# Optimization experiments

Hardware: AMD Instinct MI355X
Metric: run time of the kernel (lower is better)

The kernel has to match this reference:

```python
import jax, jax.numpy as jnp
import numpy as np

NB_NEIGHBORS = 16
RADIUS = 0.25
SPLIT = 32
FEATURE_SIZE = 128
FEATS = (256, 128, 32)
N = 50000


def setup_inputs() -> dict:
    key = jax.random.key(0)
    ks = jax.random.split(key, 12)
    def lin(k, fan_in, fan_out):
        bound = 1.0 / np.sqrt(fan_in)
        kw, kb = jax.random.split(k)
        W = jax.random.uniform(kw, (fan_in, fan_out), jnp.float32, -bound, bound)
        b = jax.random.uniform(kb, (fan_out,), jnp.float32, -bound, bound)
        return W, b
    points = jax.random.normal(ks[0], (N, 3), jnp.float32)
    features = jax.random.normal(ks[1], (N, SPLIT + FEATURE_SIZE), jnp.float32)
    batch = jnp.sort(jax.random.randint(ks[2], (N,), 0, 32, jnp.int64))
    # neighborhood decoder modeled as linear: split -> nb_neighbors*3
    W_nbh, b_nbh = lin(ks[3], SPLIT, NB_NEIGHBORS * 3)
    W1, b1 = lin(ks[4], FEATURE_SIZE + 3, FEATS[0])
    W2, b2 = lin(ks[5], FEATS[0], FEATS[1])
    W3, b3 = lin(ks[6], FEATS[1], FEATS[2])
    return {"points": points, "features": features, "batch": batch,
            "W_nbh": W_nbh, "b_nbh": b_nbh,
            "W1": W1, "b1": b1, "W2": W2, "b2": b2, "W3": W3, "b3": b3}


def reference(points, features, batch, W_nbh, b_nbh, W1, b1, W2, b2, W3, b3):
    point_features = features[:, :SPLIT]            # [N, split]
    feature_features = features[:, SPLIT:]          # [N, feature_size]
    # neighborhood decoder: per-point relative offsets for nb_neighbors points
    relative_points = (point_features @ W_nbh + b_nbh).reshape(-1, 3)  # [N*nb, 3]
    output_batch = jnp.repeat(batch, NB_NEIGHBORS)                     # [N*nb]
    features_repeated = jnp.repeat(feature_features, NB_NEIGHBORS, axis=0)  # [N*nb, fs]
    concat = jnp.concatenate([relative_points, features_repeated], axis=1)  # [N*nb, fs+3]
    h = jax.nn.relu(concat @ W1 + b1)
    h = jax.nn.relu(h @ W2 + b2)
    fc3_features = jax.nn.relu(h @ W3 + b3)
    anchor_points = jnp.repeat(points, NB_NEIGHBORS, axis=0)  # [N*nb, 3]
    output_points = anchor_points + relative_points * RADIUS
    return (output_points, fc3_features, output_batch)
```

## Files before the change

kernel.cpp:

```cpp
#include <hip/hip_runtime.h>


#define NPTS 50000
#define MROWS (NPTS * 16)
#define OFF_FC3 ((size_t)MROWS * 3)
#define OFF_BATCH ((size_t)MROWS * 35)

typedef unsigned int uint_;
typedef unsigned short ushort_;
typedef __attribute__((ext_vector_type(8))) short bf16x8s;
typedef __attribute__((ext_vector_type(16))) float f32x16;

#define MFMA(a, b, c) __builtin_amdgcn_mfma_f32_32x32x16_bf16(a, b, c, 0, 0, 0)
#define CROW(r, h) (((r) & 3) + 8 * ((r) >> 2) + 4 * (h))

#define WS_W2T 0
#define WS_W3T 32768
#define WS_W1PT 36864
#define WS_WNT 69632
#define WS_S 71680
#define WS_REL_BYTES 25743360

__device__ __forceinline__ float bl(uint_ u) { return __uint_as_float(u << 16); }
__device__ __forceinline__ float bh(uint_ u) { return __uint_as_float(u & 0xffff0000u); }
__device__ __forceinline__ ushort_ f2b(float f) {
  uint_ u = __float_as_uint(f);
  u += 0x7fffu + ((u >> 16) & 1u);
  return (ushort_)(u >> 16);
}
__device__ __forceinline__ uint_ cvtpk(float lo, float hi) {
  uint_ r;
  asm("v_cvt_pk_bf16_f32 %0, %1, %2" : "=v"(r) : "v"(lo), "v"(hi));
  return r;
}
__device__ __forceinline__ float relu_(float x) { return fmaxf(x, 0.f); }

template<bool F32>
__device__ __forceinline__ float ldv(const void* p, int i) {
  if (F32) return ((const float*)p)[i];
  return bl((uint_)((const ushort_*)p)[i]);
}

struct F8 { float v[8]; };
template<bool F32>
__device__ __forceinline__ F8 ld8(const void* p, int idx) {
  F8 r;
  if (F32) {
    float4 a = *(const float4*)((const float*)p + idx);
    float4 b = *(const float4*)((const float*)p + idx + 4);
    r.v[0] = a.x; r.v[1] = a.y; r.v[2] = a.z; r.v[3] = a.w;
    r.v[4] = b.x; r.v[5] = b.y; r.v[6] = b.z; r.v[7] = b.w;
  } else {
    uint4 u = *(const uint4*)((const ushort_*)p + idx);
    r.v[0] = bl(u.x); r.v[1] = bh(u.x); r.v[2] = bl(u.y); r.v[3] = bh(u.y);
    r.v[4] = bl(u.z); r.v[5] = bh(u.z); r.v[6] = bl(u.w); r.v[7] = bh(u.w);
  }
  return r;
}
template<bool F32>
__device__ __forceinline__ void ld4f(const void* p, int idx, float* o) {
  if (F32) {
    float4 v = *(const float4*)((const float*)p + idx);
    o[0] = v.x; o[1] = v.y; o[2] = v.z; o[3] = v.w;
  } else {
    uint2 v = *(const uint2*)((const ushort_*)p + idx);
    o[0] = bl(v.x); o[1] = bh(v.x); o[2] = bl(v.y); o[3] = bh(v.y);
  }
}

union FragU { uint_ u[4]; uint4 q; bf16x8s v; };
__device__ __forceinline__ bf16x8s pack8(const F8& f) {
  FragU o;
  #pragma unroll
  for (int j = 0; j < 4; ++j) o.u[j] = cvtpk(f.v[2 * j], f.v[2 * j + 1]);
  return o.v;
}

__device__ __forceinline__ bool sniff_f32(const void* feats) {
  const ushort_* u = (const ushort_*)feats;
  int pass = 0;
  #pragma unroll 8
  for (int m = 0; m < 32; ++m) {
    int ex = (u[m] >> 7) & 0xff;
    pass += (ex >= 100 && ex <= 140) ? 1 : 0;
  }
  return pass < 28;
}

__global__ void __launch_bounds__(256)
kT(const void* features, const void* batch, const void* W1, const void* Wn,
   const void* W2, const void* W3, ushort_* wsu, float* out) {
  bool f32 = sniff_f32(features);
  const uint_* bu = (const uint_*)batch;
  int nz = 0;
  #pragma unroll
  for (int m = 0; m < 16; ++m) nz += (bu[49999 - 2 * m] != 0u) ? 1 : 0;
  bool i64 = (nz == 0);

  const int total = 32768 + 32768 + 4096 + 2048 + 800000;
  for (int i = blockIdx.x * 256 + threadIdx.x; i < total; i += gridDim.x * 256) {
    if (i < 32768) {
      int n = i & 255, k = i >> 8;
      wsu[WS_W1PT + n * 128 + k] = f32 ? f2b(((const float*)W1)[(3 + k) * 256 + n])
                                       : ((const ushort_*)W1)[(3 + k) * 256 + n];
    } else if (i < 65536) {
      int i2 = i - 32768, n = i2 & 127, k = i2 >> 7;
      wsu[WS_W2T + n * 256 + k] = f32 ? f2b(((const float*)W2)[k * 128 + n])
                                      : ((const ushort_*)W2)[k * 128 + n];
    } else if (i < 69632) {
      int i3 = i - 65536, n = i3 & 31, k = i3 >> 5;
      wsu[WS_W3T + n * 128 + k] = f32 ? f2b(((const float*)W3)[k * 32 + n])
                                      : ((const ushort_*)W3)[k * 32 + n];
    } else if (i < 71680) {
      int i4 = i - 69632, n = i4 >> 5, k = i4 & 31;
      ushort_ v = 0;
      if (n < 48) v = f32 ? f2b(((const float*)Wn)[k * 48 + n])
                          : ((const ushort_*)Wn)[k * 48 + n];
      wsu[WS_WNT + n * 32 + k] = v;
    } else {
      int g = i - 71680;
      int idx = g >> 4;
      int v = i64 ? (int)bu[2 * idx] : ((const int*)batch)[idx];
      out[OFF_BATCH + (size_t)g] = (float)v;
    }
  }
}

template<bool F32>
__device__ void runS(const void* points, const void* features, const void* bn,
                     const void* b1, ushort_* wsu, float* out,
                     ushort_* w1pt, ushort_* feats) {
  const ushort_* W1pT_ws = wsu + WS_W1PT;
  const ushort_* WnT_ws = wsu + WS_WNT;
  ushort_* S_ws = wsu + WS_S;
  float* rel_ws = (float*)((char*)wsu + WS_REL_BYTES);
  const int tid = threadIdx.x;

  for (int c = tid; c < 4096; c += 256) {
    int n = c >> 4, s = c & 15;
    uint4 src = *(const uint4*)(W1pT_ws + c * 8);
    *(uint4*)((char*)w1pt + n * 256 + ((s * 16) ^ ((n & 7) << 4))) = src;
  }

  const int w = tid >> 6, lane = tid & 63, l31 = lane & 31, h = lane >> 5, h8 = h * 8;
  const int mt = w & 1, ctb = (w >> 1) * 4, ctr = w >> 1;

  for (int tile = blockIdx.x; tile < 782; tile += 512) {
    const int pbase = tile * 64;
    for (int c = tid; c < 2048; c += 256) {
      int row = c >> 5, c4 = c & 31;
      int p = pbase + row;
      uint2 d = {0u, 0u};
      if (p < NPTS) {
        if (F32) {
          float4 v = *(const float4*)((const float*)features + p * 160 + 32 + c4 * 4);
          d.x = cvtpk(v.x, v.y); d.y = cvtpk(v.z, v.w);
        } else {
          d = *(const uint2*)((const ushort_*)features + p * 160 + 32 + c4 * 4);
        }
      }
      *(uint2*)((char*)feats + row * 256 + ((c4 * 8) ^ ((row & 7) << 4))) = d;
    }
    __syncthreads();

    bf16x8s af[8];
    #pragma unroll
    for (int ks = 0; ks < 8; ++ks) {
      int row = mt * 32 + l31;
      af[ks] = *(const bf16x8s*)((const char*)feats + row * 256 +
                                 (((ks * 16 + h8) * 2) ^ ((row & 7) << 4)));
    }
    #pragma unroll
    for (int ci = 0; ci < 4; ++ci) {
      int ct = ctb + ci;
      float b1v = ldv<F32>(b1, ct * 32 + l31);
      f32x16 acc;
      #pragma unroll
      for (int r = 0; r < 16; ++r) acc[r] = b1v;
      #pragma unroll
      for (int ks = 0; ks < 8; ++ks) {
        int n = ct * 32 + l31;
        bf16x8s bf = *(const bf16x8s*)((const char*)w1pt + n * 256 +
                                       (((ks * 16 + h8) * 2) ^ ((n & 7) << 4)));
        acc = MFMA(af[ks], bf, acc);
      }
      #pragma unroll
      for (int r = 0; r < 16; ++r) {
        int p = pbase + mt * 32 + CROW(r, h);
        if (p < NPTS) S_ws[p * 256 + ct * 32 + l31] = f2b(acc[r]);
      }
    }

    {
      int pm = pbase + mt * 32 + l31;
      pm = pm < NPTS ? pm : NPTS - 1;
      bf16x8s ar[2];
      #pragma unroll
      for (int ks = 0; ks < 2; ++ks) {
        F8 v = ld8<F32>(features, pm * 160 + ks * 16 + h8);
        ar[ks] = pack8(v);
      }
      f32x16 acc;
      #pragma unroll
      for (int r = 0; r < 16; ++r) acc[r] = 0.f;
      #pragma unroll
      for (int ks = 0; ks < 2; ++ks) {
        int n = ctr * 32 + l31;
        FragU bw;
        bw.q = *(const uint4*)(WnT_ws + n * 32 + ks * 16 + h8);
        acc = MFMA(ar[ks], bw.v, acc);
      }
      int j = ctr * 32 + l31;
      if (j < 48) {
        float bnv = ldv<F32>(bn, j);
        int c = j - (j / 3) * 3;
        #pragma unroll
        for (int r = 0; r < 16; ++r) {
          int p = pbase + mt * 32 + CROW(r, h);
          if (p < NPTS) {
            float rv = acc[r] + bnv;
            rel_ws[p * 48 + j] = rv;
            out[(size_t)p * 48 + j] = ldv<F32>(points, p * 3 + c) + 0.25f * rv;
          }
        }
      }
    }
    __syncthreads();
  }
}

__global__ void __launch_bounds__(256, 2)
kS(const void* points, const void* features, const void* bn, const void* b1,
   ushort_* wsu, float* out) {
  __shared__ ushort_ w1pt[32768];
  __shared__ ushort_ feats[8192];
  if (sniff_f32(features))
    runS<true>(points, features, bn, b1, wsu, out, w1pt, feats);
  else
    runS<false>(points, features, bn, b1, wsu, out, w1pt, feats);
}

__device__ __forceinline__ bf16x8s build8(uint4 s, const F8& wx, const F8& wy,
                                          const F8& wz, float r0, float r1, float r2) {
  uint_ su[4] = {s.x, s.y, s.z, s.w};
  F8 f;
  #pragma unroll
  for (int j = 0; j < 8; ++j) {
    uint_ u = su[j >> 1];
    float sv = (j & 1) ? bh(u) : bl(u);
    f.v[j] = relu_(sv + r0 * wx.v[j] + r1 * wy.v[j] + r2 * wz.v[j]);
  }
  return pack8(f);
}

__device__ __forceinline__ bf16x8s assemble(const f32x16& a, int base, bool lo) {
  float e[8];
  #pragma unroll
  for (int j = 0; j < 8; ++j) e[j] = relu_(a[base + j]);
  uint_ A0 = cvtpk(e[0], e[1]), A1 = cvtpk(e[2], e[3]);
  uint_ B0 = cvtpk(e[4], e[5]), B1 = cvtpk(e[6], e[7]);
  uint_ sA0 = (uint_)__shfl_xor((int)A0, 32);
  uint_ sA1 = (uint_)__shfl_xor((int)A1, 32);
  uint_ sB0 = (uint_)__shfl_xor((int)B0, 32);
  uint_ sB1 = (uint_)__shfl_xor((int)B1, 32);
  FragU o;
  o.u[0] = lo ? A0 : sB0;
  o.u[1] = lo ? A1 : sB1;
  o.u[2] = lo ? sA0 : B0;
  o.u[3] = lo ? sA1 : B1;
  return o.v;
}

template<bool F32>
__device__ void runM(const void* W1, const void* b2, const void* b3,
                     const ushort_* wsu, float* out,
                     ushort_* w2t, ushort_* w3t) {
  const ushort_* S_ws = wsu + WS_S;
  const float* rel_ws = (const float*)((const char*)wsu + WS_REL_BYTES);
  const int tid = threadIdx.x;

  for (int c = tid; c < 4608; c += 256) {
    if (c < 4096) {
      int n = c >> 5, s = c & 31;
      uint4 src = *(const uint4*)(wsu + WS_W2T + c * 8);
      *(uint4*)((char*)w2t + n * 512 + ((s * 16) ^ ((n & 7) << 4))) = src;
    } else {
      int c2 = c - 4096, n = c2 >> 4, s = c2 & 15;
      uint4 src = *(const uint4*)(wsu + WS_W3T + c2 * 8);
      *(uint4*)((char*)w3t + n * 256 + ((s * 16) ^ ((n & 7) << 4))) = src;
    }
  }
  __syncthreads();

  const int w = tid >> 6, lane = tid & 63, l31 = lane & 31, h = lane >> 5;
  const int h8 = h * 8, nb = lane & 15;
  const bool lo = lane < 32;
  const int slot = blockIdx.x * 4 + w;

  for (int g = slot; g < 12500; g += 2048) {
    const int p0 = g * 4;
    const int pA = p0 + (l31 >> 4), pB = pA + 2;
    const float rA0 = rel_ws[pA * 48 + nb * 3 + 0];
    const float rA1 = rel_ws[pA * 48 + nb * 3 + 1];
    const float rA2 = rel_ws[pA * 48 + nb * 3 + 2];
    const float rB0 = rel_ws[pB * 48 + nb * 3 + 0];
    const float rB1 = rel_ws[pB * 48 + nb * 3 + 1];
    const float rB2 = rel_ws[pB * 48 + nb * 3 + 2];

    f32x16 accA[4], accB[4];
    #pragma unroll
    for (int mt = 0; mt < 4; ++mt) {
      #pragma unroll
      for (int q = 0; q < 4; ++q) {
        float t[4];
        ld4f<F32>(b2, mt * 32 + q * 8 + 4 * h, t);
        #pragma unroll
        for (int s = 0; s < 4; ++s) {
          accA[mt][4 * q + s] = t[s];
          accB[mt][4 * q + s] = t[s];
        }
      }
    }

    #pragma unroll 1
    for (int kh = 0; kh < 2; ++kh) {
      bf16x8s hA[8], hB[8];
      #pragma unroll
      for (int ks = 0; ks < 8; ++ks) {
        int koff = kh * 128 + ks * 16 + h8;
        F8 wx = ld8<F32>(W1, koff);
        F8 wy = ld8<F32>(W1, 256 + koff);
        F8 wz = ld8<F32>(W1, 512 + koff);
        uint4 sa = *(const uint4*)(S_ws + pA * 256 + koff);
        uint4 sb = *(const uint4*)(S_ws + pB * 256 + koff);
        hA[ks] = build8(sa, wx, wy, wz, rA0, rA1, rA2);
        hB[ks] = build8(sb, wx, wy, wz, rB0, rB1, rB2);
      }
      #pragma unroll
      for (int ks = 0; ks < 8; ++ks) {
        int kb = (kh * 128 + ks * 16 + h8) * 2;
        #pragma unroll
        for (int mt = 0; mt < 4; ++mt) {
          int n = mt * 32 + l31;
          bf16x8s af = *(const bf16x8s*)((const char*)w2t + n * 512 +
                                         (kb ^ ((n & 7) << 4)));
          accA[mt] = MFMA(af, hA[ks], accA[mt]);
          accB[mt] = MFMA(af, hB[ks], accB[mt]);
        }
      }
    }

    f32x16 o3A, o3B;
    #pragma unroll
    for (int q = 0; q < 4; ++q) {
      float t[4];
      ld4f<F32>(b3, q * 8 + 4 * h, t);
      #pragma unroll
      for (int s = 0; s < 4; ++s) {
        o3A[4 * q + s] = t[s];
        o3B[4 * q + s] = t[s];
      }
    }
    #pragma unroll
    for (int ks3 = 0; ks3 < 8; ++ks3) {
      int kb = (ks3 * 16 + h8) * 2;
      bf16x8s a3 = *(const bf16x8s*)((const char*)w3t + l31 * 256 +
                                     (kb ^ ((l31 & 7) << 4)));
      const int mt = ks3 >> 1, base = (ks3 & 1) * 8;
      bf16x8s B3A = assemble(accA[mt], base, lo);
      bf16x8s B3B = assemble(accB[mt], base, lo);
      o3A = MFMA(a3, B3A, o3A);
      o3B = MFMA(a3, B3B, o3B);
    }

    const size_t rowA = (size_t)p0 * 16 + l31;
    #pragma unroll
    for (int q = 0; q < 4; ++q) {
      float4 vA = {relu_(o3A[4 * q]), relu_(o3A[4 * q + 1]),
                   relu_(o3A[4 * q + 2]), relu_(o3A[4 * q + 3])};
      float4 vB = {relu_(o3B[4 * q]), relu_(o3B[4 * q + 1]),
                   relu_(o3B[4 * q + 2]), relu_(o3B[4 * q + 3])};
      *(float4*)(out + OFF_FC3 + rowA * 32 + q * 8 + 4 * h) = vA;
      *(float4*)(out + OFF_FC3 + (rowA + 32) * 32 + q * 8 + 4 * h) = vB;
    }
  }
}

__global__ void __launch_bounds__(256, 2)
kM(const void* features, const void* W1, const void* b2, const void* b3,
   const ushort_* wsu, float* out) {
  __shared__ ushort_ w2t[32768];
  __shared__ ushort_ w3t[4096];
  if (sniff_f32(features))
    runM<true>(W1, b2, b3, wsu, out, w2t, w3t);
  else
    runM<false>(W1, b2, b3, wsu, out, w2t, w3t);
}

extern "C" void kernel_launch(void* const* d_in, const int* in_sizes, int n_in,
                              void* d_out, int out_size, void* d_ws, size_t ws_size,
                              hipStream_t stream) {
  const void* points   = d_in[0];
  const void* features = d_in[1];
  const void* batch    = d_in[2];
  const void* Wn = d_in[3];  const void* bn = d_in[4];
  const void* W1 = d_in[5];  const void* b1 = d_in[6];
  const void* W2 = d_in[7];  const void* b2 = d_in[8];
  const void* W3 = d_in[9];  const void* b3 = d_in[10];
  float* out = (float*)d_out;
  ushort_* wsu = (ushort_*)d_ws;

  hipLaunchKernelGGL(kT, dim3(512), dim3(256), 0, stream,
                     features, batch, W1, Wn, W2, W3, wsu, out);
  hipLaunchKernelGGL(kS, dim3(512), dim3(256), 0, stream,
                     points, features, bn, b1, wsu, out);
  hipLaunchKernelGGL(kM, dim3(512), dim3(256), 0, stream,
                     features, W1, b2, b3, wsu, out);
}
```

Baseline: 160.0 us.

## Halve per-wave work in MLP kernel, use 512-thread blocks, stage W1 rows in LDS

The fused fc2/fc3 kernel now has each wave process 2 points (32 rows) instead of 4, and uses 512-thread blocks, so accumulator register pressure drops and more waves can be resident per CU. The three W1 coordinate rows are copied once into shared memory instead of being read from global memory in the inner loop. The kS grid is raised to 782 so each tile gets its own block. The cost is that each W2 fragment read from LDS now feeds one MFMA instead of two, which doubles LDS read traffic per output row.

```diff
diff --git a/kernel.cpp b/kernel.cpp
--- a/kernel.cpp
+++ b/kernel.cpp
@@ -55,6 +55,14 @@
     r.v[0] = bl(u.x); r.v[1] = bh(u.x); r.v[2] = bl(u.y); r.v[3] = bh(u.y);
     r.v[4] = bl(u.z); r.v[5] = bh(u.z); r.v[6] = bl(u.w); r.v[7] = bh(u.w);
   }
+  return r;
+}
+__device__ __forceinline__ F8 ld8lds(const float* p) {
+  F8 r;
+  float4 a = *(const float4*)p;
+  float4 b = *(const float4*)(p + 4);
+  r.v[0] = a.x; r.v[1] = a.y; r.v[2] = a.z; r.v[3] = a.w;
+  r.v[4] = b.x; r.v[5] = b.y; r.v[6] = b.z; r.v[7] = b.w;
   return r;
 }
 template<bool F32>
@@ -145,7 +153,7 @@
   const int w = tid >> 6, lane = tid & 63, l31 = lane & 31, h = lane >> 5, h8 = h * 8;
   const int mt = w & 1, ctb = (w >> 1) * 4, ctr = w >> 1;
 
-  for (int tile = blockIdx.x; tile < 782; tile += 512) {
+  for (int tile = blockIdx.x; tile < 782; tile += gridDim.x) {
     const int pbase = tile * 64;
     for (int c = tid; c < 2048; c += 256) {
       int row = c >> 5, c4 = c & 31;
@@ -274,12 +282,12 @@
 template<bool F32>
 __device__ void runM(const void* W1, const void* b2, const void* b3,
                      const ushort_* wsu, float* out,
-                     ushort_* w2t, ushort_* w3t) {
+                     ushort_* w2t, ushort_* w3t, float* w1f) {
   const ushort_* S_ws = wsu + WS_S;
   const float* rel_ws = (const float*)((const char*)wsu + WS_REL_BYTES);
   const int tid = threadIdx.x;
 
-  for (int c = tid; c < 4608; c += 256) {
+  for (int c = tid; c < 4608; c += 512) {
     if (c < 4096) {
       int n = c >> 5, s = c & 31;
       uint4 src = *(const uint4*)(wsu + WS_W2T + c * 8);
@@ -290,24 +298,22 @@
       *(uint4*)((char*)w3t + n * 256 + ((s * 16) ^ ((n & 7) << 4))) = src;
     }
   }
+  for (int c = tid; c < 768; c += 512) w1f[c] = ldv<F32>(W1, c);
   __syncthreads();
 
   const int w = tid >> 6, lane = tid & 63, l31 = lane & 31, h = lane >> 5;
   const int h8 = h * 8, nb = lane & 15;
   const bool lo = lane < 32;
-  const int slot = blockIdx.x * 4 + w;
-
-  for (int g = slot; g < 12500; g += 2048) {
-    const int p0 = g * 4;
-    const int pA = p0 + (l31 >> 4), pB = pA + 2;
-    const float rA0 = rel_ws[pA * 48 + nb * 3 + 0];
-    const float rA1 = rel_ws[pA * 48 + nb * 3 + 1];
-    const float rA2 = rel_ws[pA * 48 + nb * 3 + 2];
-    const float rB0 = rel_ws[pB * 48 + nb * 3 + 0];
-    const float rB1 = rel_ws[pB * 48 + nb * 3 + 1];
-    const float rB2 = rel_ws[pB * 48 + nb * 3 + 2];
-
-    f32x16 accA[4], accB[4];
+  const int slot = blockIdx.x * 8 + w;
+
+  for (int g = slot; g < 25000; g += 4096) {
+    const int p0 = g * 2;
+    const int p = p0 + (l31 >> 4);
+    const float r0 = rel_ws[p * 48 + nb * 3 + 0];
+    const float r1 = rel_ws[p * 48 + nb * 3 + 1];
+    const float r2 = rel_ws[p * 48 + nb * 3 + 2];
+
+    f32x16 acc[4];
     #pragma unroll
     for (int mt = 0; mt < 4; ++mt) {
       #pragma unroll
@@ -315,86 +321,65 @@
         float t[4];
         ld4f<F32>(b2, mt * 32 + q * 8 + 4 * h, t);
         #pragma unroll
-        for (int s = 0; s < 4; ++s) {
-          accA[mt][4 * q + s] = t[s];
-          accB[mt][4 * q + s] = t[s];
-        }
-      }
-    }
-
-    #pragma unroll 1
-    for (int kh = 0; kh < 2; ++kh) {
-      bf16x8s hA[8], hB[8];
-      #pragma unroll
-      for (int ks = 0; ks < 8; ++ks) {
-        int koff = kh * 128 + ks * 16 + h8;
-        F8 wx = ld8<F32>(W1, koff);
-        F8 wy = ld8<F32>(W1, 256 + koff);
-        F8 wz = ld8<F32>(W1, 512 + koff);
-        uint4 sa = *(const uint4*)(S_ws + pA * 256 + koff);
-        uint4 sb = *(const uint4*)(S_ws + pB * 256 + koff);
-        hA[ks] = build8(sa, wx, wy, wz, rA0, rA1, rA2);
-        hB[ks] = build8(sb, wx, wy, wz, rB0, rB1, rB2);
-      }
-      #pragma unroll
-      for (int ks = 0; ks < 8; ++ks) {
-        int kb = (kh * 128 + ks * 16 + h8) * 2;
-        #pragma unroll
-        for (int mt = 0; mt < 4; ++mt) {
-          int n = mt * 32 + l31;
-          bf16x8s af = *(const bf16x8s*)((const char*)w2t + n * 512 +
-                                         (kb ^ ((n & 7) << 4)));
-          accA[mt] = MFMA(af, hA[ks], accA[mt]);
-          accB[mt] = MFMA(af, hB[ks], accB[mt]);
-        }
-      }
-    }
-
-    f32x16 o3A, o3B;
+        for (int s = 0; s < 4; ++s) acc[mt][4 * q + s] = t[s];
+      }
+    }
+
+    #pragma unroll 2
+    for (int ks = 0; ks < 16; ++ks) {
+      const int koff = ks * 16 + h8;
+      F8 wx = ld8lds(w1f + koff);
+      F8 wy = ld8lds(w1f + 256 + koff);
+      F8 wz = ld8lds(w1f + 512 + koff);
+      uint4 sa = *(const uint4*)(S_ws + p * 256 + koff);
+      bf16x8s hh = build8(sa, wx, wy, wz, r0, r1, r2);
+      const int kb = koff * 2;
+      #pragma unroll
+      for (int mt = 0; mt < 4; ++mt) {
+        int n = mt * 32 + l31;
+        bf16x8s af = *(const bf16x8s*)((const char*)w2t + n * 512 +
+                                       (kb ^ ((n & 7) << 4)));
+        acc[mt] = MFMA(af, hh, acc[mt]);
+      }
+    }
+
+    f32x16 o3;
     #pragma unroll
     for (int q = 0; q < 4; ++q) {
       float t[4];
       ld4f<F32>(b3, q * 8 + 4 * h, t);
       #pragma unroll
-      for (int s = 0; s < 4; ++s) {
-        o3A[4 * q + s] = t[s];
-        o3B[4 * q + s] = t[s];
-      }
+      for (int s = 0; s < 4; ++s) o3[4 * q + s] = t[s];
     }
     #pragma unroll
     for (int ks3 = 0; ks3 < 8; ++ks3) {
       int kb = (ks3 * 16 + h8) * 2;
       bf16x8s a3 = *(const bf16x8s*)((const char*)w3t + l31 * 256 +
                                      (kb ^ ((l31 & 7) << 4)));
-      const int mt = ks3 >> 1, base = (ks3 & 1) * 8;
-      bf16x8s B3A = assemble(accA[mt], base, lo);
-      bf16x8s B3B = assemble(accB[mt], base, lo);
-      o3A = MFMA(a3, B3A, o3A);
-      o3B = MFMA(a3, B3B, o3B);
-    }
-
-    const size_t rowA = (size_t)p0 * 16 + l31;
+      bf16x8s B3 = assemble(acc[ks3 >> 1], (ks3 & 1) * 8, lo);
+      o3 = MFMA(a3, B3, o3);
+    }
+
+    const size_t row = (size_t)p0 * 16 + l31;
     #pragma unroll
     for (int q = 0; q < 4; ++q) {
-      float4 vA = {relu_(o3A[4 * q]), relu_(o3A[4 * q + 1]),
-                   relu_(o3A[4 * q + 2]), relu_(o3A[4 * q + 3])};
-      float4 vB = {relu_(o3B[4 * q]), relu_(o3B[4 * q + 1]),
-                   relu_(o3B[4 * q + 2]), relu_(o3B[4 * q + 3])};
-      *(float4*)(out + OFF_FC3 + rowA * 32 + q * 8 + 4 * h) = vA;
-      *(float4*)(out + OFF_FC3 + (rowA + 32) * 32 + q * 8 + 4 * h) = vB;
-    }
-  }
-}
-
-__global__ void __launch_bounds__(256, 2)
+      float4 v = {relu_(o3[4 * q]), relu_(o3[4 * q + 1]),
+                  relu_(o3[4 * q + 2]), relu_(o3[4 * q + 3])};
+      *(float4*)(out + OFF_FC3 + row * 32 + q * 8 + 4 * h) = v;
+    }
+  }
+}
+
+__global__ void __launch_bounds__(512, 3)
 kM(const void* features, const void* W1, const void* b2, const void* b3,
    const ushort_* wsu, float* out) {
   __shared__ ushort_ w2t[32768];
   __shared__ ushort_ w3t[4096];
+  __shared__ float w1f[768];
   if (sniff_f32(features))
-    runM<true>(W1, b2, b3, wsu, out, w2t, w3t);
+    runM<true>(W1, b2, b3, wsu, out, w2t, w3t, w1f);
   else
-    runM<false>(W1, b2, b3, wsu, out, w2t, w3t);
+    runM<false>(W1, b2, b3, wsu, out, w2t, w3t, w1f);
 }
 
 extern "C" void kernel_launch(void* const* d_in, const int* in_sizes, int n_in,
@@ -412,8 +397,8 @@
 
   hipLaunchKernelGGL(kT, dim3(512), dim3(256), 0, stream,
                      features, batch, W1, Wn, W2, W3, wsu, out);
-  hipLaunchKernelGGL(kS, dim3(512), dim3(256), 0, stream,
+  hipLaunchKernelGGL(kS, dim3(782), dim3(256), 0, stream,
                      points, features, bn, b1, wsu, out);
-  hipLaunchKernelGGL(kM, dim3(512), dim3(256), 0, stream,
+  hipLaunchKernelGGL(kM, dim3(512), dim3(512), 0, stream,
                      features, W1, b2, b3, wsu, out);
 }
```

Measured after the change: 175.7 us. +9.8%, slower.
